# Kernel optimization log

Measured on AMD Instinct MI355X. Metric: run time of the kernel, lower is better.

## Reference

```python
import jax, jax.numpy as jnp
import numpy as np

N = 4096   # nodes
G = 64     # graphs
MH = 128   # hidden multiplicity (0e and 1o)
MU = 64    # up multiplicity (0e and 1o)
NSP = 10   # num_species
EPS = 1e-5


def _forward(nfh, nfu, onehot, W_h0, W_h1, W_u0, W_u1, Wt_00, Wt_11, Wt_01, Wt_10,
             W_p0, b_p0, W_p1, Wsc0, Wsc1, ln_w0, ln_b0, ln_w1, W_s0, b_s0, W_s1, batch):
    n = nfh.shape[0]
    # unpack irreps layout: [0e scalars | 1o vectors flattened]
    h0 = nfh[:, :MH]                       # [N, MH]
    h1 = nfh[:, MH:].reshape(n, MH, 3)     # [N, MH, 3]
    u0 = nfu[:, :MU]
    u1 = nfu[:, MU:].reshape(n, MU, 3)
    inv_h = 1.0 / np.sqrt(MH)
    inv_u = 1.0 / np.sqrt(MU)
    # irrep-wise (block-diagonal) o3.Linear, e3nn fan-in normalization
    hp0 = (h0 @ W_h0) * inv_h
    hp1 = jnp.einsum('nui,uv->nvi', h1, W_h1) * inv_h
    up0 = (u0 @ W_u0) * inv_u
    up1 = jnp.einsum('nui,uv->nvi', u1, W_u1) * inv_u
    # SeparateWeightTensorProduct: fully-connected 'uvw' CG tensor product
    # paths to 0e (scalars + gates, 2*MH outputs): 0e x 0e and 1o x 1o (dot / sqrt3)
    inv_tp = 1.0 / np.sqrt(2.0 * MH * MU)   # component/path normalization (2 paths, fan MH*MU)
    xy00 = jnp.einsum('nu,nv->nuv', hp0, up0).reshape(n, MH * MU)
    xy11 = jnp.einsum('nui,nvi->nuv', hp1, up1).reshape(n, MH * MU)
    z0 = (xy00 @ Wt_00.reshape(MH * MU, 2 * MH)
          + (xy11 @ Wt_11.reshape(MH * MU, 2 * MH)) / np.sqrt(3.0)) * inv_tp  # [N, 2*MH]
    # paths to 1o: 0e x 1o and 1o x 0e (staged to control intermediate size)
    ta = jnp.einsum('nu,uvw->nvw', hp0, Wt_01)       # [N, MU, MH]
    z1a = jnp.einsum('nvw,nvi->nwi', ta, up1)
    tb = jnp.einsum('nv,uvw->nuw', up0, Wt_10)       # [N, MH, MH]
    z1b = jnp.einsum('nuw,nui->nwi', tb, hp1)
    z1 = (z1a + z1b) * inv_tp                        # [N, MH, 3]
    # Gate nonlinearity: silu on scalars, sigmoid gates multiply 1o features
    s = jax.nn.silu(z0[:, :MH])
    g = jax.nn.sigmoid(z0[:, MH:])
    v = z1 * g[:, :, None]
    # lin_post (biases on scalars only)
    p0 = (s @ W_p0) * inv_h + b_p0
    p1 = jnp.einsum('nui,uv->nvi', v, W_p1) * inv_h
    # self-connection: FullyConnectedTensorProduct(hidden, NSPx0e, out)
    inv_sc = 1.0 / np.sqrt(MH * NSP)
    sxy0 = jnp.einsum('nu,nv->nuv', h0, onehot).reshape(n, MH * NSP)
    y0 = p0 + (sxy0 @ Wsc0.reshape(MH * NSP, MH)) * inv_sc
    sxy1 = jnp.einsum('nui,nv->nuvi', h1, onehot).reshape(n, MH * NSP, 3)
    y1 = p1 + jnp.einsum('nki,kw->nwi', sxy1, Wsc1.reshape(MH * NSP, MH)) * inv_sc
    # e3LayerNorm: per-graph stats; mean-subtract scalars only, RMS-normalize per irrep
    ones = jnp.ones((n,), y0.dtype)
    cnt = jnp.maximum(jax.ops.segment_sum(ones, batch, num_segments=G), 1.0)[:, None]
    mean0 = (jax.ops.segment_sum(y0, batch, num_segments=G) / cnt).mean(axis=1)  # [G]
    f0 = y0 - mean0[batch][:, None]
    var0 = (jax.ops.segment_sum(f0 * f0, batch, num_segments=G) / cnt).mean(axis=1)
    f0 = f0 / (jnp.sqrt(var0)[batch][:, None] + EPS) * ln_w0 + ln_b0
    var1 = (jax.ops.segment_sum((y1 * y1).reshape(n, -1), batch, num_segments=G) / cnt).mean(axis=1)
    f1 = y1 / (jnp.sqrt(var1)[batch][:, None, None] + EPS) * ln_w1[None, :, None]
    # residual skip connection (o3.Linear with scalar bias)
    out0 = f0 + (h0 @ W_s0) * inv_h + b_s0
    out1 = f1 + jnp.einsum('nui,uv->nvi', h1, W_s1) * inv_h
    return jnp.concatenate([out0, out1.reshape(n, 3 * MH)], axis=1)  # [N, 512]


def setup_inputs() -> dict:
    key = jax.random.key(0)
    ks = jax.random.split(key, 20)
    f = lambda i, shape: jax.random.normal(ks[i], shape, dtype=jnp.float32)
    species = jax.random.randint(ks[0], (N,), 0, NSP)
    return {
        'node_feats_hidden': f(1, (N, 4 * MH)),
        'node_feats_up': f(2, (N, 4 * MU)),
        'node_one_hot': jax.nn.one_hot(species, NSP, dtype=jnp.float32),
        'batch': jnp.sort(jax.random.randint(ks[3], (N,), 0, G)),
        'W_h0': f(4, (MH, MH)), 'W_h1': f(5, (MH, MH)),
        'W_u0': f(6, (MU, MU)), 'W_u1': f(7, (MU, MU)),
        'Wt_00': f(8, (MH, MU, 2 * MH)), 'Wt_11': f(9, (MH, MU, 2 * MH)),
        'Wt_01': f(10, (MH, MU, MH)), 'Wt_10': f(11, (MH, MU, MH)),
        'W_p0': f(12, (MH, MH)), 'b_p0': jnp.zeros((MH,), jnp.float32), 'W_p1': f(13, (MH, MH)),
        'Wsc0': f(14, (MH, NSP, MH)), 'Wsc1': f(15, (MH, NSP, MH)),
        'ln_w0': jnp.ones((MH,), jnp.float32), 'ln_b0': jnp.zeros((MH,), jnp.float32),
        'ln_w1': jnp.ones((MH,), jnp.float32),
        'W_s0': f(16, (MH, MH)), 'b_s0': jnp.zeros((MH,), jnp.float32), 'W_s1': f(17, (MH, MH)),
    }


def reference(node_feats_hidden, node_feats_up, node_one_hot, batch, W_h0, W_h1, W_u0, W_u1,
              Wt_00, Wt_11, Wt_01, Wt_10, W_p0, b_p0, W_p1, Wsc0, Wsc1, ln_w0, ln_b0, ln_w1,
              W_s0, b_s0, W_s1):
    return _forward(node_feats_hidden, node_feats_up, node_one_hot, W_h0, W_h1, W_u0, W_u1,
                    Wt_00, Wt_11, Wt_01, Wt_10, W_p0, b_p0, W_p1, Wsc0, Wsc1,
                    ln_w0, ln_b0, ln_w1, W_s0, b_s0, W_s1, batch)
```

## Files before the change

kernel.cpp:

```cpp
#include <hip/hip_runtime.h>
#include <cstdint>
#include <cstddef>


typedef _Float16 half8 __attribute__((ext_vector_type(8)));
typedef _Float16 half4v __attribute__((ext_vector_type(4)));
typedef float f32x4 __attribute__((ext_vector_type(4)));

static constexpr float INV_H  = 0.08838834764831845f;
static constexpr float INV_U  = 0.125f;
static constexpr float INV_TP = 0.0078125f;
static constexpr float INV_SC = 0.02795084971874737f;
static constexpr float RSQRT3 = 0.5773502691896258f;
static constexpr float LN_EPS = 1e-5f;

static constexpr size_t OFF_BZ0 = 0;
static constexpr size_t OFF_BZ1 = OFF_BZ0 + 8388608;
static constexpr size_t OFF_WH0 = OFF_BZ1 + 4194304;
static constexpr size_t OFF_WH1 = OFF_WH0 + 32768;
static constexpr size_t OFF_WU0 = OFF_WH1 + 32768;
static constexpr size_t OFF_WU1 = OFF_WU0 + 8192;
static constexpr size_t OFF_WP0 = OFF_WU1 + 8192;
static constexpr size_t OFF_WP1 = OFF_WP0 + 32768;
static constexpr size_t OFF_WS0 = OFF_WP1 + 32768;
static constexpr size_t OFF_WS1 = OFF_WS0 + 32768;
static constexpr size_t OFF_H0F = OFF_WS1 + 32768;
static constexpr size_t OFF_H1F = OFF_H0F + 1048576;
static constexpr size_t OFF_U0F = OFF_H1F + 3145728;
static constexpr size_t OFF_U1F = OFF_U0F + 524288;
static constexpr size_t OFF_HP0 = OFF_U1F + 1572864;
static constexpr size_t OFF_HP1 = OFF_HP0 + 1048576;
static constexpr size_t OFF_UP0 = OFF_HP1 + 3145728;
static constexpr size_t OFF_UP1 = OFF_UP0 + 524288;
static constexpr size_t OFF_SF  = OFF_UP1 + 1572864;
static constexpr size_t OFF_VF  = OFF_SF + 1048576;
static constexpr size_t OFF_PZ0 = OFF_VF + 3145728;
static constexpr size_t OFF_PZ1 = OFF_PZ0 + 16777216;
static constexpr size_t OFF_Y0  = OFF_PZ1 + 12582912;
static constexpr size_t OFF_Y1  = OFF_Y0 + 2097152;
static constexpr size_t OFF_O0  = OFF_Y1 + 6291456;
static constexpr size_t OFF_O1  = OFF_O0 + 2097152;
static constexpr size_t OFF_SP  = OFF_O1 + 6291456;
static constexpr size_t OFF_ST  = OFF_SP + 16384;
static constexpr size_t WS_NEED = OFF_ST + 2048;

__global__ __launch_bounds__(256) void kconv(
    const float* __restrict__ nfh, const float* __restrict__ nfu,
    const float* __restrict__ onehot,
    const float* __restrict__ Wt00, const float* __restrict__ Wt11,
    const float* __restrict__ Wt01, const float* __restrict__ Wt10,
    const float* __restrict__ Wh0, const float* __restrict__ Wh1,
    const float* __restrict__ Wu0, const float* __restrict__ Wu1,
    const float* __restrict__ Wp0, const float* __restrict__ Wp1,
    const float* __restrict__ Ws0, const float* __restrict__ Ws1,
    char* __restrict__ ws)
{
  const int bid = blockIdx.x, t = threadIdx.x;
  if (bid < 768) {
    _Float16* dst;
    int u, nt = 0;
    const bool isz0 = bid < 512;
    if (isz0) { nt = bid >> 8; u = bid & 255; dst = (_Float16*)(ws + OFF_BZ0) + ((size_t)nt*256 + (size_t)u)*8192; }
    else      { u = bid - 512;               dst = (_Float16*)(ws + OFF_BZ1) + (size_t)u*8192; }
    for (int it = 0; it < 4; ++it) {
      int chunk = it*256 + t;
      int lane = chunk & 63, ch = chunk >> 6;
      int f = ch >> 1, c = ch & 1;
      int w = f*16 + (lane & 15);
      int v0 = c*32 + (lane >> 4)*8;
      half8 o;
      #pragma unroll
      for (int j = 0; j < 8; ++j) {
        float val;
        if (isz0) {
          if (u < 128) val = Wt00[(size_t)((u*64 + v0 + j)*256) + nt*128 + w];
          else         val = Wt11[(size_t)(((u-128)*64 + v0 + j)*256) + nt*128 + w] * RSQRT3;
        } else {
          if (u < 128) val = Wt01[(size_t)((u*64 + v0 + j)*128) + w];
          else         val = Wt10[(size_t)(((u-128)*64 + v0 + j)*128) + w];
        }
        o[j] = (_Float16)val;
      }
      *(half8*)(dst + (size_t)chunk*8) = o;
    }
  } else if (bid < 776) {
    int mat = bid - 768;
    const float* src; size_t doff; int K, N;
    switch (mat) {
      case 0: src = Wh0; doff = OFF_WH0; K = 128; N = 128; break;
      case 1: src = Wh1; doff = OFF_WH1; K = 128; N = 128; break;
      case 2: src = Wu0; doff = OFF_WU0; K = 64;  N = 64;  break;
      case 3: src = Wu1; doff = OFF_WU1; K = 64;  N = 64;  break;
      case 4: src = Wp0; doff = OFF_WP0; K = 128; N = 128; break;
      case 5: src = Wp1; doff = OFF_WP1; K = 128; N = 128; break;
      case 6: src = Ws0; doff = OFF_WS0; K = 128; N = 128; break;
      default: src = Ws1; doff = OFF_WS1; K = 128; N = 128; break;
    }
    _Float16* d = (_Float16*)(ws + doff);
    const int nfr = N >> 4;
    const int chunks = (K*N) >> 3;
    for (int qd = t; qd < chunks; qd += 256) {
      int lane = qd & 63, cf = qd >> 6;
      int f = cf % nfr, c = cf / nfr;
      int col = f*16 + (lane & 15);
      int k0 = c*32 + (lane >> 4)*8;
      half8 o;
      #pragma unroll
      for (int j = 0; j < 8; ++j) o[j] = (_Float16)src[(size_t)(k0 + j)*N + col];
      *(half8*)(d + (size_t)qd*8) = o;
    }
  } else if (bid < 1544) {
    const int stride = 768*256;
    const int base = (bid - 776)*256 + t;
    _Float16* h0f = (_Float16*)(ws + OFF_H0F);
    _Float16* h1f = (_Float16*)(ws + OFF_H1F);
    _Float16* u0f = (_Float16*)(ws + OFF_U0F);
    _Float16* u1f = (_Float16*)(ws + OFF_U1F);
    for (int id = base; id < 524288; id += stride)
      h0f[id] = (_Float16)nfh[(size_t)(id >> 7)*512 + (id & 127)];
    for (int id = base; id < 1572864; id += stride) {
      int i = id >> 19, r = id & 524287, n = r >> 7, u = r & 127;
      h1f[id] = (_Float16)nfh[(size_t)n*512 + 128 + u*3 + i];
    }
    for (int id = base; id < 262144; id += stride)
      u0f[id] = (_Float16)nfu[(size_t)(id >> 6)*256 + (id & 63)];
    for (int id = base; id < 786432; id += stride) {
      int i = id >> 18, r = id & 262143, n = r >> 6, v = r & 63;
      u1f[id] = (_Float16)nfu[(size_t)n*256 + 64 + v*3 + i];
    }
  } else {
    int node = (bid - 1544)*256 + t;
    const float* row = onehot + (size_t)node*10;
    int best = 0; float bv = row[0];
    #pragma unroll
    for (int s = 1; s < 10; ++s) { float v = row[s]; if (v > bv) { bv = v; best = s; } }
    ((int*)(ws + OFF_SP))[node] = best;
    if (bid == 1544) {
      float* stz = (float*)(ws + OFF_ST);
      stz[t] = 0.f; stz[t + 256] = 0.f;
    }
  }
}

template<int KK, int NO, int MODE>
__global__ __launch_bounds__(256) void kgemm_small(char* __restrict__ ws,
    const float* __restrict__ bp0, const float* __restrict__ bs0)
{
  constexpr int NT = NO / 16;
  const int bid = blockIdx.x, t = threadIdx.x;
  const int lane = t & 63, wid = t >> 6;
  const int quad = lane >> 4, l15 = lane & 15;
  const int job = bid >> 5, n0 = (bid & 31) << 7;

  const _Float16 *A, *W;
  _Float16* oh = nullptr; float* of = nullptr;
  const float* bias = nullptr;
  float scale;
  if constexpr (MODE == 0) {
    scale = INV_H;
    if (job == 0) { A = (const _Float16*)(ws + OFF_H0F); W = (const _Float16*)(ws + OFF_WH0); oh = (_Float16*)(ws + OFF_HP0); }
    else {
      A = (const _Float16*)(ws + OFF_H1F) + (size_t)(job-1)*524288;
      W = (const _Float16*)(ws + OFF_WH1);
      oh = (_Float16*)(ws + OFF_HP1) + (size_t)(job-1)*524288;
    }
  } else if constexpr (MODE == 1) {
    scale = INV_U;
    if (job == 0) { A = (const _Float16*)(ws + OFF_U0F); W = (const _Float16*)(ws + OFF_WU0); oh = (_Float16*)(ws + OFF_UP0); }
    else {
      A = (const _Float16*)(ws + OFF_U1F) + (size_t)(job-1)*262144;
      W = (const _Float16*)(ws + OFF_WU1);
      oh = (_Float16*)(ws + OFF_UP1) + (size_t)(job-1)*262144;
    }
  } else {
    scale = INV_H;
    switch (job) {
      case 0: A = (const _Float16*)(ws + OFF_SF);  W = (const _Float16*)(ws + OFF_WP0); of = (float*)(ws + OFF_Y0); bias = bp0; break;
      case 1: A = (const _Float16*)(ws + OFF_H0F); W = (const _Float16*)(ws + OFF_WS0); of = (float*)(ws + OFF_O0); bias = bs0; break;
      case 2: case 3: case 4:
        A = (const _Float16*)(ws + OFF_VF) + (size_t)(job-2)*524288;
        W = (const _Float16*)(ws + OFF_WP1);
        of = (float*)(ws + OFF_Y1) + (size_t)(job-2)*524288; break;
      default:
        A = (const _Float16*)(ws + OFF_H1F) + (size_t)(job-5)*524288;
        W = (const _Float16*)(ws + OFF_WS1);
        of = (float*)(ws + OFF_O1) + (size_t)(job-5)*524288; break;
    }
  }

  f32x4 acc[2][NT];
  const f32x4 zz = {0.f, 0.f, 0.f, 0.f};
  #pragma unroll
  for (int mf = 0; mf < 2; ++mf)
    #pragma unroll
    for (int nf = 0; nf < NT; ++nf) acc[mf][nf] = zz;

  #pragma unroll
  for (int kc = 0; kc < KK/32; ++kc) {
    half8 a[2];
    #pragma unroll
    for (int mf = 0; mf < 2; ++mf)
      a[mf] = *(const half8*)(A + (size_t)(n0 + wid*32 + mf*16 + l15)*KK + kc*32 + quad*8);
    #pragma unroll
    for (int nf = 0; nf < NT; ++nf) {
      half8 b = *(const half8*)(W + (size_t)(kc*NT + nf)*512 + lane*8);
      #pragma unroll
      for (int mf = 0; mf < 2; ++mf)
        acc[mf][nf] = __builtin_amdgcn_mfma_f32_16x16x32_f16(a[mf], b, acc[mf][nf], 0, 0, 0);
    }
  }

  #pragma unroll
  for (int mf = 0; mf < 2; ++mf)
    #pragma unroll
    for (int nf = 0; nf < NT; ++nf) {
      int col = nf*16 + l15;
      float bv = bias ? bias[col] : 0.f;
      #pragma unroll
      for (int r = 0; r < 4; ++r) {
        int row = n0 + wid*32 + mf*16 + quad*4 + r;
        float v = acc[mf][nf][r] * scale + bv;
        if constexpr (MODE < 2) oh[(size_t)row*NO + col] = (_Float16)v;
        else                    of[(size_t)row*NO + col] = v;
      }
    }
}

__global__ __launch_bounds__(256, 2) void kbig(char* __restrict__ ws)
{
  const int bid = blockIdx.x, t = threadIdx.x;
  const int lane = t & 63, wid = t >> 6;
  const int wy = wid >> 1, wx = wid & 1;
  const int quad = lane >> 4, l15 = lane & 15;

  const _Float16* hp0 = (const _Float16*)(ws + OFF_HP0);
  const _Float16* hp1 = (const _Float16*)(ws + OFF_HP1);
  const _Float16* up0 = (const _Float16*)(ws + OFF_UP0);
  const _Float16* up1 = (const _Float16*)(ws + OFF_UP1);

  const _Float16 *p, *q, *B0;
  float* out; int opitch; size_t obase; int node0;
  if (bid < 256) {
    int mt = bid >> 3, nt = (bid >> 2) & 1, kj = bid & 3;
    node0 = mt << 7;
    if (kj == 0) { p = hp0; q = up0; }
    else { p = hp1 + (size_t)(kj-1)*524288; q = up1 + (size_t)(kj-1)*262144; }
    B0 = (const _Float16*)(ws + OFF_BZ0) + (size_t)nt*2097152 + (kj ? (size_t)1048576 : (size_t)0);
    out = (float*)(ws + OFF_PZ0) + (size_t)kj*1048576;
    obase = (size_t)node0*256 + (size_t)nt*128;
    opitch = 256;
  } else {
    int b2 = bid - 256, mt = b2 >> 1, kj = b2 & 1, i = mt >> 5;
    node0 = (mt & 31) << 7;
    if (kj == 0) { p = hp0; q = up1 + (size_t)i*262144; }
    else         { p = hp1 + (size_t)i*524288; q = up0; }
    B0 = (const _Float16*)(ws + OFF_BZ1) + (kj ? (size_t)1048576 : (size_t)0);
    out = (float*)(ws + OFF_PZ1) + (size_t)kj*1572864;
    obase = (size_t)mt*16384;
    opitch = 128;
  }

  half8 qf[4][2];
  #pragma unroll
  for (int mf = 0; mf < 4; ++mf)
    #pragma unroll
    for (int c = 0; c < 2; ++c)
      qf[mf][c] = *(const half8*)(q + (size_t)(node0 + wy*64 + mf*16 + l15)*64 + c*32 + quad*8);

  f32x4 acc[4][4];
  const f32x4 zz = {0.f, 0.f, 0.f, 0.f};
  #pragma unroll
  for (int mf = 0; mf < 4; ++mf)
    #pragma unroll
    for (int nf = 0; nf < 4; ++nf) acc[mf][nf] = zz;

  const _Float16* prow = p + (size_t)(node0 + wy*64 + l15)*128;
  const _Float16* Bw = B0 + (size_t)wx*4096 + (size_t)lane*8;

  auto loadB = [&](half8 (&dst)[2][4], int uidx) {
    const _Float16* Bu = Bw + (size_t)uidx*8192;
    #pragma unroll
    for (int c = 0; c < 2; ++c)
      #pragma unroll
      for (int nf = 0; nf < 4; ++nf)
        dst[c][nf] = *(const half8*)(Bu + (size_t)((nf*2 + c)*512));
  };
  auto mstep = [&](const half8 (&bf)[2][4], const half4v (&pwl)[4], int uu) {
    #pragma unroll
    for (int mf = 0; mf < 4; ++mf) {
      const _Float16 ps = pwl[mf][uu];
      const half8 pv = {ps, ps, ps, ps, ps, ps, ps, ps};
      #pragma unroll
      for (int c = 0; c < 2; ++c) {
        half8 a = qf[mf][c] * pv;
        #pragma unroll
        for (int nf = 0; nf < 4; ++nf)
          acc[mf][nf] = __builtin_amdgcn_mfma_f32_16x16x32_f16(a, bf[c][nf], acc[mf][nf], 0, 0, 0);
      }
    }
  };

  half4v pw[4], pwN[4];
  #pragma unroll
  for (int mf = 0; mf < 4; ++mf)
    pw[mf] = *(const half4v*)(prow + (size_t)mf*2048);

  half8 bfA[2][4], bfB[2][4];
  loadB(bfA, 0);

  for (int u4 = 0; u4 < 32; ++u4) {
    const int b = u4*4;
    loadB(bfB, b + 1);
    mstep(bfA, pw, 0);
    loadB(bfA, b + 2);
    mstep(bfB, pw, 1);
    {
      const int np = (u4 < 31) ? (u4 + 1)*4 : u4*4;
      #pragma unroll
      for (int mf = 0; mf < 4; ++mf)
        pwN[mf] = *(const half4v*)(prow + (size_t)mf*2048 + np);
    }
    loadB(bfB, b + 3);
    mstep(bfA, pw, 2);
    loadB(bfA, (u4 < 31) ? (b + 4) : (b + 3));
    mstep(bfB, pw, 3);
    #pragma unroll
    for (int mf = 0; mf < 4; ++mf) pw[mf] = pwN[mf];
  }

  #pragma unroll
  for (int mf = 0; mf < 4; ++mf)
    #pragma unroll
    for (int nf = 0; nf < 4; ++nf) {
      int col = wx*64 + nf*16 + l15;
      #pragma unroll
      for (int r = 0; r < 4; ++r) {
        int row = wy*64 + mf*16 + quad*4 + r;
        out[obase + (size_t)row*opitch + col] = acc[mf][nf][r];
      }
    }
}

__global__ __launch_bounds__(256) void kreduce(char* __restrict__ ws)
{
  const int id = blockIdx.x*256 + threadIdx.x;
  const int n = id >> 7, w = id & 127;
  const float* pz0 = (const float*)(ws + OFF_PZ0);
  const float* pz1 = (const float*)(ws + OFF_PZ1);
  _Float16* sf = (_Float16*)(ws + OFF_SF);
  _Float16* vf = (_Float16*)(ws + OFF_VF);
  const size_t b = (size_t)n*256;
  float zs = (pz0[b + w] + pz0[1048576 + b + w] + pz0[2097152 + b + w] + pz0[3145728 + b + w]) * INV_TP;
  float zg = (pz0[b + 128 + w] + pz0[1048576 + b + 128 + w] + pz0[2097152 + b + 128 + w] + pz0[3145728 + b + 128 + w]) * INV_TP;
  float s = zs / (1.f + __expf(-zs));
  float g = 1.f / (1.f + __expf(-zg));
  sf[id] = (_Float16)s;
  #pragma unroll
  for (int i = 0; i < 3; ++i) {
    size_t r = ((size_t)i*4096 + (size_t)n)*128 + w;
    float z1v = (pz1[r] + pz1[1572864 + r]) * INV_TP;
    vf[(size_t)i*524288 + (size_t)n*128 + w] = (_Float16)(z1v * g);
  }
}

__global__ __launch_bounds__(256) void kscstats(char* __restrict__ ws,
    const float* __restrict__ nfh,
    const float* __restrict__ Wsc0, const float* __restrict__ Wsc1,
    const int* __restrict__ batch)
{
  const int t = threadIdx.x;
  const int node = blockIdx.x*2 + (t >> 7);
  const int w = t & 127;
  const int sp = ((const int*)(ws + OFF_SP))[node];
  const float* h = nfh + (size_t)node*512;
  float a0 = 0.f, a10 = 0.f, a11 = 0.f, a12 = 0.f;
  for (int u = 0; u < 128; ++u) {
    const size_t wi = (size_t)(u*10 + sp)*128 + w;
    float w0 = Wsc0[wi];
    float w1 = Wsc1[wi];
    a0 += h[u] * w0;
    a10 += h[128 + u*3 + 0] * w1;
    a11 += h[128 + u*3 + 1] * w1;
    a12 += h[128 + u*3 + 2] * w1;
  }
  float* y0 = (float*)(ws + OFF_Y0);
  float* y1 = (float*)(ws + OFF_Y1);
  const size_t i0 = (size_t)node*128 + w;
  float y0n  = y0[i0]           + INV_SC * a0;
  float y1n0 = y1[i0]           + INV_SC * a10;
  float y1n1 = y1[524288 + i0]  + INV_SC * a11;
  float y1n2 = y1[1048576 + i0] + INV_SC * a12;
  y0[i0] = y0n;
  y1[i0] = y1n0;
  y1[524288 + i0]  = y1n1;
  y1[1048576 + i0] = y1n2;

  float s0 = y0n, ss0 = y0n*y0n, ss1 = y1n0*y1n0 + y1n1*y1n1 + y1n2*y1n2;
  #pragma unroll
  for (int m = 1; m < 64; m <<= 1) {
    s0  += __shfl_xor(s0, m, 64);
    ss0 += __shfl_xor(ss0, m, 64);
    ss1 += __shfl_xor(ss1, m, 64);
  }
  __shared__ float red[4][3];
  if ((t & 63) == 0) {
    red[t >> 6][0] = s0; red[t >> 6][1] = ss0; red[t >> 6][2] = ss1;
  }
  __syncthreads();
  if ((t & 127) == 0) {
    const int wv = t >> 6;
    float* stp = (float*)(ws + OFF_ST);
    const int g = batch[node];
    atomicAdd(&stp[g],       red[wv][0] + red[wv+1][0]);
    atomicAdd(&stp[64 + g],  red[wv][1] + red[wv+1][1]);
    atomicAdd(&stp[128 + g], red[wv][2] + red[wv+1][2]);
    atomicAdd(&stp[192 + g], 1.f);
  }
}

__global__ __launch_bounds__(256) void kfinal(char* __restrict__ ws, const int* __restrict__ batch,
    const float* __restrict__ lnw0, const float* __restrict__ lnb0, const float* __restrict__ lnw1,
    float* __restrict__ outp)
{
  const int id = blockIdx.x*256 + threadIdx.x;
  const int n = id >> 9, c = id & 511;
  const float* st = (const float*)(ws + OFF_ST);
  const int g = batch[n];
  const float cnt = fmaxf(st[192 + g], 1.f);
  float val;
  if (c < 128) {
    const float* y0 = (const float*)(ws + OFF_Y0);
    const float* o0 = (const float*)(ws + OFF_O0);
    float m0   = st[g] / (cnt * 128.f);
    float var0 = st[64 + g] / (cnt * 128.f) - m0*m0;
    float inv0 = 1.f / (sqrtf(fmaxf(var0, 0.f)) + LN_EPS);
    val = (y0[(size_t)n*128 + c] - m0) * inv0 * lnw0[c] + lnb0[c] + o0[(size_t)n*128 + c];
  } else {
    int cc = c - 128, w = cc / 3, i = cc - w*3;
    const float* y1 = (const float*)(ws + OFF_Y1);
    const float* o1 = (const float*)(ws + OFF_O1);
    float inv1 = 1.f / (sqrtf(fmaxf(st[128 + g] / (cnt * 384.f), 0.f)) + LN_EPS);
    val = y1[(size_t)i*524288 + (size_t)n*128 + w] * inv1 * lnw1[w]
        + o1[(size_t)i*524288 + (size_t)n*128 + w];
  }
  outp[id] = val;
}

extern "C" void kernel_launch(void* const* d_in, const int* in_sizes, int n_in,
                              void* d_out, int out_size, void* d_ws, size_t ws_size,
                              hipStream_t stream)
{
  const float* nfh   = (const float*)d_in[0];
  const float* nfu   = (const float*)d_in[1];
  const float* oneh  = (const float*)d_in[2];
  const int*   batch = (const int*)d_in[3];
  const float* Wh0   = (const float*)d_in[4];
  const float* Wh1   = (const float*)d_in[5];
  const float* Wu0   = (const float*)d_in[6];
  const float* Wu1   = (const float*)d_in[7];
  const float* Wt00  = (const float*)d_in[8];
  const float* Wt11  = (const float*)d_in[9];
  const float* Wt01  = (const float*)d_in[10];
  const float* Wt10  = (const float*)d_in[11];
  const float* Wp0   = (const float*)d_in[12];
  const float* bp0   = (const float*)d_in[13];
  const float* Wp1   = (const float*)d_in[14];
  const float* Wsc0  = (const float*)d_in[15];
  const float* Wsc1  = (const float*)d_in[16];
  const float* lnw0  = (const float*)d_in[17];
  const float* lnb0  = (const float*)d_in[18];
  const float* lnw1  = (const float*)d_in[19];
  const float* Ws0   = (const float*)d_in[20];
  const float* bs0   = (const float*)d_in[21];
  const float* Ws1   = (const float*)d_in[22];
  char* ws = (char*)d_ws;

  if (ws_size < WS_NEED) {
    hipMemsetAsync(d_out, 0, (size_t)out_size * sizeof(float), stream);
    return;
  }

  kconv<<<1560, 256, 0, stream>>>(nfh, nfu, oneh, Wt00, Wt11, Wt01, Wt10,
                                  Wh0, Wh1, Wu0, Wu1, Wp0, Wp1, Ws0, Ws1, ws);
  kgemm_small<128,128,0><<<128, 256, 0, stream>>>(ws, nullptr, nullptr);
  kgemm_small<64, 64, 1><<<128, 256, 0, stream>>>(ws, nullptr, nullptr);
  kbig<<<448, 256, 0, stream>>>(ws);
  kreduce<<<2048, 256, 0, stream>>>(ws);
  kgemm_small<128,128,2><<<256, 256, 0, stream>>>(ws, bp0, bs0);
  kscstats<<<2048, 256, 0, stream>>>(ws, nfh, Wsc0, Wsc1, batch);
  kfinal<<<8192, 256, 0, stream>>>(ws, batch, lnw0, lnb0, lnw1, (float*)d_out);
}
```

Baseline: 353.8 us.

## Restructure big tensor-product GEMM to share B tiles across spatial planes with K-split

Rewrites the main tensor-product kernel as a templated worker that processes all three vector components (planes) per B-fragment load, so each weight tile is reused across planes instead of reloaded per component. The K dimension is split in two with partial sums written to separate buffers, which the reduce kernel now adds together, and the grid grows from 448 to 640 blocks. The explicit double-buffered B prefetch is dropped in favour of simpler per-step loads. This trades more accumulator registers and extra partial-sum traffic for fewer weight loads and more parallelism.

```diff
diff --git a/kernel.cpp b/kernel.cpp
--- a/kernel.cpp
+++ b/kernel.cpp
@@ -226,119 +226,147 @@
     }
 }
 
+template<int MF, int NF, int PLANES, int PN, int QN, bool Z0>
+__device__ __forceinline__ void bigwork(
+    const _Float16* p0, const _Float16* p1, const _Float16* p2,
+    const _Float16* q0, const _Float16* q1, const _Float16* q2,
+    const _Float16* Bt,
+    float* out, size_t obase, int opitch,
+    int node0, int ks, int fbase, int t)
+{
+  constexpr int ACCP  = Z0 ? 1 : PLANES;
+  constexpr int WROWS = MF * 16;
+  const int lane = t & 63;
+  const int wy = (t >> 7) & 1;
+  const int quad = lane >> 4, l15 = lane & 15;
+
+  const _Float16* pp[3] = {p0, p1, p2};
+  const _Float16* qq[3] = {q0, q1, q2};
+
+  half8 qf[QN][MF][2];
+  #pragma unroll
+  for (int qi = 0; qi < QN; ++qi)
+    #pragma unroll
+    for (int mf = 0; mf < MF; ++mf)
+      #pragma unroll
+      for (int c = 0; c < 2; ++c)
+        qf[qi][mf][c] = *(const half8*)(qq[qi] + (size_t)(node0 + wy*WROWS + mf*16 + l15)*64 + c*32 + quad*8);
+
+  f32x4 acc[ACCP][MF][NF];
+  const f32x4 zz = {0.f, 0.f, 0.f, 0.f};
+  #pragma unroll
+  for (int ap = 0; ap < ACCP; ++ap)
+    #pragma unroll
+    for (int mf = 0; mf < MF; ++mf)
+      #pragma unroll
+      for (int nf = 0; nf < NF; ++nf) acc[ap][mf][nf] = zz;
+
+  const _Float16* prow[PN];
+  #pragma unroll
+  for (int pi = 0; pi < PN; ++pi)
+    prow[pi] = pp[pi] + (size_t)(node0 + wy*WROWS + l15)*128 + ks*64;
+
+  const _Float16* Bl = Bt + (size_t)fbase*1024 + (size_t)lane*8;
+
+  for (int u4 = 0; u4 < 16; ++u4) {
+    half4v pw[PN][MF];
+    #pragma unroll
+    for (int pi = 0; pi < PN; ++pi)
+      #pragma unroll
+      for (int mf = 0; mf < MF; ++mf)
+        pw[pi][mf] = *(const half4v*)(prow[pi] + (size_t)mf*2048 + u4*4);
+    #pragma unroll
+    for (int uu = 0; uu < 4; ++uu) {
+      const _Float16* Bu = Bl + (size_t)(u4*4 + uu)*8192;
+      half8 bf[2][NF];
+      #pragma unroll
+      for (int c = 0; c < 2; ++c)
+        #pragma unroll
+        for (int nf = 0; nf < NF; ++nf)
+          bf[c][nf] = *(const half8*)(Bu + (size_t)((nf*2 + c)*512));
+      #pragma unroll
+      for (int c = 0; c < 2; ++c)
+        #pragma unroll
+        for (int pl = 0; pl < PLANES; ++pl)
+          #pragma unroll
+          for (int mf = 0; mf < MF; ++mf) {
+            const _Float16 ps = pw[PN == 1 ? 0 : pl][mf][uu];
+            const half8 pv = {ps, ps, ps, ps, ps, ps, ps, ps};
+            half8 a = qf[QN == 1 ? 0 : pl][mf][c] * pv;
+            #pragma unroll
+            for (int nf = 0; nf < NF; ++nf)
+              acc[Z0 ? 0 : pl][mf][nf] =
+                __builtin_amdgcn_mfma_f32_16x16x32_f16(a, bf[c][nf], acc[Z0 ? 0 : pl][mf][nf], 0, 0, 0);
+          }
+    }
+  }
+
+  #pragma unroll
+  for (int pl = 0; pl < ACCP; ++pl)
+    #pragma unroll
+    for (int mf = 0; mf < MF; ++mf)
+      #pragma unroll
+      for (int nf = 0; nf < NF; ++nf) {
+        const int col = (fbase + nf)*16 + l15;
+        #pragma unroll
+        for (int r = 0; r < 4; ++r) {
+          const int row = wy*WROWS + mf*16 + quad*4 + r;
+          out[(size_t)pl*524288 + obase + (size_t)row*opitch + col] = acc[pl][mf][nf][r];
+        }
+      }
+}
+
 __global__ __launch_bounds__(256, 2) void kbig(char* __restrict__ ws)
 {
   const int bid = blockIdx.x, t = threadIdx.x;
-  const int lane = t & 63, wid = t >> 6;
-  const int wy = wid >> 1, wx = wid & 1;
-  const int quad = lane >> 4, l15 = lane & 15;
+  const int wx = (t >> 6) & 1;
 
   const _Float16* hp0 = (const _Float16*)(ws + OFF_HP0);
   const _Float16* hp1 = (const _Float16*)(ws + OFF_HP1);
   const _Float16* up0 = (const _Float16*)(ws + OFF_UP0);
   const _Float16* up1 = (const _Float16*)(ws + OFF_UP1);
-
-  const _Float16 *p, *q, *B0;
-  float* out; int opitch; size_t obase; int node0;
-  if (bid < 256) {
-    int mt = bid >> 3, nt = (bid >> 2) & 1, kj = bid & 3;
-    node0 = mt << 7;
-    if (kj == 0) { p = hp0; q = up0; }
-    else { p = hp1 + (size_t)(kj-1)*524288; q = up1 + (size_t)(kj-1)*262144; }
-    B0 = (const _Float16*)(ws + OFF_BZ0) + (size_t)nt*2097152 + (kj ? (size_t)1048576 : (size_t)0);
-    out = (float*)(ws + OFF_PZ0) + (size_t)kj*1048576;
-    obase = (size_t)node0*256 + (size_t)nt*128;
-    opitch = 256;
+  const _Float16* BZ0h = (const _Float16*)(ws + OFF_BZ0);
+  const _Float16* BZ1h = (const _Float16*)(ws + OFF_BZ1);
+  float* pz0 = (float*)(ws + OFF_PZ0);
+  float* pzA = (float*)(ws + OFF_PZ1);
+  float* pzB = (float*)(ws + OFF_Y0);
+
+  if (bid < 128) {
+    const int idx = bid, mt = idx >> 3, nb = (idx >> 1) & 3, ks = idx & 1;
+    const int node0 = mt << 8, nt = nb >> 1;
+    const int fbase = (nb & 1)*4 + wx*2;
+    const _Float16* Bt = BZ0h + (size_t)(nt*256 + ks*64)*8192;
+    bigwork<8, 2, 1, 1, 1, true>(hp0, hp0, hp0, up0, up0, up0, Bt,
+        pz0 + (size_t)ks*1048576, (size_t)node0*256 + (size_t)nt*128, 256,
+        node0, ks, fbase, t);
+  } else if (bid < 384) {
+    const int idx = bid - 128, mt = idx >> 3, cb = (idx >> 1) & 3, ks = idx & 1;
+    const int node0 = mt << 7, nt = cb >> 1;
+    const int fbase = (cb & 1)*4 + wx*2;
+    const _Float16* Bt = BZ0h + (size_t)(nt*256 + 128 + ks*64)*8192;
+    bigwork<4, 2, 3, 3, 3, true>(hp1, hp1 + 524288, hp1 + 1048576,
+                                 up1, up1 + 262144, up1 + 524288, Bt,
+        pz0 + (size_t)(2 + ks)*1048576, (size_t)node0*256 + (size_t)nt*128, 256,
+        node0, ks, fbase, t);
+  } else if (bid < 512) {
+    const int idx = bid - 384, mt = idx >> 2, nb = (idx >> 1) & 1, ks = idx & 1;
+    const int node0 = mt << 7;
+    const int fbase = nb*4 + wx*2;
+    const _Float16* Bt = BZ1h + (size_t)(ks*64)*8192;
+    bigwork<4, 2, 3, 1, 3, false>(hp0, hp0, hp0,
+                                  up1, up1 + 262144, up1 + 524288, Bt,
+        pzA + (size_t)ks*1572864, (size_t)node0*128, 128,
+        node0, ks, fbase, t);
   } else {
-    int b2 = bid - 256, mt = b2 >> 1, kj = b2 & 1, i = mt >> 5;
-    node0 = (mt & 31) << 7;
-    if (kj == 0) { p = hp0; q = up1 + (size_t)i*262144; }
-    else         { p = hp1 + (size_t)i*524288; q = up0; }
-    B0 = (const _Float16*)(ws + OFF_BZ1) + (kj ? (size_t)1048576 : (size_t)0);
-    out = (float*)(ws + OFF_PZ1) + (size_t)kj*1572864;
-    obase = (size_t)mt*16384;
-    opitch = 128;
-  }
-
-  half8 qf[4][2];
-  #pragma unroll
-  for (int mf = 0; mf < 4; ++mf)
-    #pragma unroll
-    for (int c = 0; c < 2; ++c)
-      qf[mf][c] = *(const half8*)(q + (size_t)(node0 + wy*64 + mf*16 + l15)*64 + c*32 + quad*8);
-
-  f32x4 acc[4][4];
-  const f32x4 zz = {0.f, 0.f, 0.f, 0.f};
-  #pragma unroll
-  for (int mf = 0; mf < 4; ++mf)
-    #pragma unroll
-    for (int nf = 0; nf < 4; ++nf) acc[mf][nf] = zz;
-
-  const _Float16* prow = p + (size_t)(node0 + wy*64 + l15)*128;
-  const _Float16* Bw = B0 + (size_t)wx*4096 + (size_t)lane*8;
-
-  auto loadB = [&](half8 (&dst)[2][4], int uidx) {
-    const _Float16* Bu = Bw + (size_t)uidx*8192;
-    #pragma unroll
-    for (int c = 0; c < 2; ++c)
-      #pragma unroll
-      for (int nf = 0; nf < 4; ++nf)
-        dst[c][nf] = *(const half8*)(Bu + (size_t)((nf*2 + c)*512));
-  };
-  auto mstep = [&](const half8 (&bf)[2][4], const half4v (&pwl)[4], int uu) {
-    #pragma unroll
-    for (int mf = 0; mf < 4; ++mf) {
-      const _Float16 ps = pwl[mf][uu];
-      const half8 pv = {ps, ps, ps, ps, ps, ps, ps, ps};
-      #pragma unroll
-      for (int c = 0; c < 2; ++c) {
-        half8 a = qf[mf][c] * pv;
-        #pragma unroll
-        for (int nf = 0; nf < 4; ++nf)
-          acc[mf][nf] = __builtin_amdgcn_mfma_f32_16x16x32_f16(a, bf[c][nf], acc[mf][nf], 0, 0, 0);
-      }
-    }
-  };
-
-  half4v pw[4], pwN[4];
-  #pragma unroll
-  for (int mf = 0; mf < 4; ++mf)
-    pw[mf] = *(const half4v*)(prow + (size_t)mf*2048);
-
-  half8 bfA[2][4], bfB[2][4];
-  loadB(bfA, 0);
-
-  for (int u4 = 0; u4 < 32; ++u4) {
-    const int b = u4*4;
-    loadB(bfB, b + 1);
-    mstep(bfA, pw, 0);
-    loadB(bfA, b + 2);
-    mstep(bfB, pw, 1);
-    {
-      const int np = (u4 < 31) ? (u4 + 1)*4 : u4*4;
-      #pragma unroll
-      for (int mf = 0; mf < 4; ++mf)
-        pwN[mf] = *(const half4v*)(prow + (size_t)mf*2048 + np);
-    }
-    loadB(bfB, b + 3);
-    mstep(bfA, pw, 2);
-    loadB(bfA, (u4 < 31) ? (b + 4) : (b + 3));
-    mstep(bfB, pw, 3);
-    #pragma unroll
-    for (int mf = 0; mf < 4; ++mf) pw[mf] = pwN[mf];
-  }
-
-  #pragma unroll
-  for (int mf = 0; mf < 4; ++mf)
-    #pragma unroll
-    for (int nf = 0; nf < 4; ++nf) {
-      int col = wx*64 + nf*16 + l15;
-      #pragma unroll
-      for (int r = 0; r < 4; ++r) {
-        int row = wy*64 + mf*16 + quad*4 + r;
-        out[obase + (size_t)row*opitch + col] = acc[mf][nf][r];
-      }
-    }
+    const int idx = bid - 512, mt = idx >> 2, nb = (idx >> 1) & 1, ks = idx & 1;
+    const int node0 = mt << 7;
+    const int fbase = nb*4 + wx*2;
+    const _Float16* Bt = BZ1h + (size_t)(128 + ks*64)*8192;
+    bigwork<4, 2, 3, 3, 1, false>(hp1, hp1 + 524288, hp1 + 1048576,
+                                  up0, up0, up0, Bt,
+        pzB + (size_t)ks*1572864, (size_t)node0*128, 128,
+        node0, ks, fbase, t);
+  }
 }
 
 __global__ __launch_bounds__(256) void kreduce(char* __restrict__ ws)
@@ -346,7 +374,8 @@
   const int id = blockIdx.x*256 + threadIdx.x;
   const int n = id >> 7, w = id & 127;
   const float* pz0 = (const float*)(ws + OFF_PZ0);
-  const float* pz1 = (const float*)(ws + OFF_PZ1);
+  const float* pzA = (const float*)(ws + OFF_PZ1);
+  const float* pzB = (const float*)(ws + OFF_Y0);
   _Float16* sf = (_Float16*)(ws + OFF_SF);
   _Float16* vf = (_Float16*)(ws + OFF_VF);
   const size_t b = (size_t)n*256;
@@ -358,7 +387,7 @@
   #pragma unroll
   for (int i = 0; i < 3; ++i) {
     size_t r = ((size_t)i*4096 + (size_t)n)*128 + w;
-    float z1v = (pz1[r] + pz1[1572864 + r]) * INV_TP;
+    float z1v = (pzA[r] + pzA[1572864 + r] + pzB[r] + pzB[1572864 + r]) * INV_TP;
     vf[(size_t)i*524288 + (size_t)n*128 + w] = (_Float16)(z1v * g);
   }
 }
@@ -484,7 +513,7 @@
                                   Wh0, Wh1, Wu0, Wu1, Wp0, Wp1, Ws0, Ws1, ws);
   kgemm_small<128,128,0><<<128, 256, 0, stream>>>(ws, nullptr, nullptr);
   kgemm_small<64, 64, 1><<<128, 256, 0, stream>>>(ws, nullptr, nullptr);
-  kbig<<<448, 256, 0, stream>>>(ws);
+  kbig<<<640, 256, 0, stream>>>(ws);
   kreduce<<<2048, 256, 0, stream>>>(ws);
   kgemm_small<128,128,2><<<256, 256, 0, stream>>>(ws, bp0, bs0);
   kscstats<<<2048, 256, 0, stream>>>(ws, nfh, Wsc0, Wsc1, batch);
```

New measurement: 370.8 us. 4.8% more time.

## Split-K the z0 GEMM blocks, remap kbig by XCD, merge small GEMM launches

Applied to the files above, without the earlier changes.

The z0 contraction blocks in kbig are split along the reduction dimension into two halves. The second half writes partial sums into the reused Y0/O0 buffers, and kreduce sums the extra partials. Block indices are remapped so that work sharing the same B weights lands on the same XCD, and the launch grows from 448 to 704 blocks. Occupancy is raised to 3 blocks per CU, and the manual double-buffered B prefetch is dropped for a simpler loop. The two prep GEMM launches are merged into one kernel. The changes target tail imbalance and L2 locality, at the cost of more partial-sum traffic and possibly exposed load latency.

```diff
diff --git a/kernel.cpp b/kernel.cpp
--- a/kernel.cpp
+++ b/kernel.cpp
@@ -143,11 +143,11 @@
 }
 
 template<int KK, int NO, int MODE>
-__global__ __launch_bounds__(256) void kgemm_small(char* __restrict__ ws,
-    const float* __restrict__ bp0, const float* __restrict__ bs0)
+__device__ __forceinline__ void gemm_small_body(char* __restrict__ ws,
+    const float* __restrict__ bp0, const float* __restrict__ bs0,
+    int bid, int t)
 {
   constexpr int NT = NO / 16;
-  const int bid = blockIdx.x, t = threadIdx.x;
   const int lane = t & 63, wid = t >> 6;
   const int quad = lane >> 4, l15 = lane & 15;
   const int job = bid >> 5, n0 = (bid & 31) << 7;
@@ -226,119 +226,131 @@
     }
 }
 
-__global__ __launch_bounds__(256, 2) void kbig(char* __restrict__ ws)
-{
-  const int bid = blockIdx.x, t = threadIdx.x;
+__global__ __launch_bounds__(256) void kprep(char* __restrict__ ws)
+{
+  if (blockIdx.x < 128) gemm_small_body<128,128,0>(ws, nullptr, nullptr, blockIdx.x, threadIdx.x);
+  else                  gemm_small_body<64, 64, 1>(ws, nullptr, nullptr, blockIdx.x - 128, threadIdx.x);
+}
+
+__global__ __launch_bounds__(256) void ktail(char* __restrict__ ws,
+    const float* __restrict__ bp0, const float* __restrict__ bs0)
+{
+  gemm_small_body<128,128,2>(ws, bp0, bs0, blockIdx.x, threadIdx.x);
+}
+
+__device__ __forceinline__ void bigloop(
+    const _Float16* __restrict__ p, const _Float16* __restrict__ q,
+    const _Float16* __restrict__ B0,
+    float* __restrict__ out, size_t obase, int opitch,
+    int node0, int ustart4, int nu4, int t)
+{
   const int lane = t & 63, wid = t >> 6;
   const int wy = wid >> 1, wx = wid & 1;
   const int quad = lane >> 4, l15 = lane & 15;
+
+  half8 qf[4][2];
+  #pragma unroll
+  for (int mf = 0; mf < 4; ++mf)
+    #pragma unroll
+    for (int c = 0; c < 2; ++c)
+      qf[mf][c] = *(const half8*)(q + (size_t)(node0 + wy*64 + mf*16 + l15)*64 + c*32 + quad*8);
+
+  f32x4 acc[4][4];
+  const f32x4 zz = {0.f, 0.f, 0.f, 0.f};
+  #pragma unroll
+  for (int mf = 0; mf < 4; ++mf)
+    #pragma unroll
+    for (int nf = 0; nf < 4; ++nf) acc[mf][nf] = zz;
+
+  const _Float16* prow = p + (size_t)(node0 + wy*64 + l15)*128 + ustart4*4;
+  const _Float16* Bw = B0 + (size_t)ustart4*32768 + (size_t)wx*4096 + (size_t)lane*8;
+
+  for (int u4 = 0; u4 < nu4; ++u4) {
+    half4v pw[4];
+    #pragma unroll
+    for (int mf = 0; mf < 4; ++mf)
+      pw[mf] = *(const half4v*)(prow + (size_t)mf*2048 + u4*4);
+    #pragma unroll
+    for (int uu = 0; uu < 4; ++uu) {
+      const _Float16* Bu = Bw + (size_t)(u4*4 + uu)*8192;
+      half8 bf[2][4];
+      #pragma unroll
+      for (int c = 0; c < 2; ++c)
+        #pragma unroll
+        for (int nf = 0; nf < 4; ++nf)
+          bf[c][nf] = *(const half8*)(Bu + (size_t)((nf*2 + c)*512));
+      #pragma unroll
+      for (int mf = 0; mf < 4; ++mf) {
+        const _Float16 ps = pw[mf][uu];
+        const half8 pv = {ps, ps, ps, ps, ps, ps, ps, ps};
+        #pragma unroll
+        for (int c = 0; c < 2; ++c) {
+          half8 a = qf[mf][c] * pv;
+          #pragma unroll
+          for (int nf = 0; nf < 4; ++nf)
+            acc[mf][nf] = __builtin_amdgcn_mfma_f32_16x16x32_f16(a, bf[c][nf], acc[mf][nf], 0, 0, 0);
+        }
+      }
+    }
+  }
+
+  #pragma unroll
+  for (int mf = 0; mf < 4; ++mf)
+    #pragma unroll
+    for (int nf = 0; nf < 4; ++nf) {
+      int col = wx*64 + nf*16 + l15;
+      #pragma unroll
+      for (int r = 0; r < 4; ++r) {
+        int row = wy*64 + mf*16 + quad*4 + r;
+        out[obase + (size_t)row*opitch + col] = acc[mf][nf][r];
+      }
+    }
+}
+
+__global__ __launch_bounds__(256, 3) void kbig(char* __restrict__ ws)
+{
+  const int bid = blockIdx.x, t = threadIdx.x;
+  const int xcd = bid & 7, j = bid >> 3;
 
   const _Float16* hp0 = (const _Float16*)(ws + OFF_HP0);
   const _Float16* hp1 = (const _Float16*)(ws + OFF_HP1);
   const _Float16* up0 = (const _Float16*)(ws + OFF_UP0);
   const _Float16* up1 = (const _Float16*)(ws + OFF_UP1);
-
-  const _Float16 *p, *q, *B0;
-  float* out; int opitch; size_t obase; int node0;
-  if (bid < 256) {
-    int mt = bid >> 3, nt = (bid >> 2) & 1, kj = bid & 3;
-    node0 = mt << 7;
+  const _Float16* BZ0 = (const _Float16*)(ws + OFF_BZ0);
+  const _Float16* BZ1 = (const _Float16*)(ws + OFF_BZ1);
+
+  if (j < 24) {
+    const int kj = xcd >> 2;
+    const int g = (xcd & 3)*24 + j;
+    const int i = g >> 5, mt = g & 31;
+    const int node0 = mt << 7;
+    const _Float16 *p, *q;
+    if (kj == 0) { p = hp0; q = up1 + (size_t)i*262144; }
+    else         { p = hp1 + (size_t)i*524288; q = up0; }
+    const _Float16* B0 = BZ1 + (kj ? (size_t)1048576 : (size_t)0);
+    float* out = (float*)(ws + OFF_PZ1) + (size_t)kj*1572864;
+    bigloop(p, q, B0, out, (size_t)(i*32 + mt)*16384, 128, node0, 0, 32, t);
+  } else {
+    const int s = xcd & 3, nt = s >> 1, ks = s & 1;
+    const int j2 = j - 24;
+    int kj, mt;
+    if (j2 < 48) {
+      const int g = (xcd >> 2)*48 + j2;
+      kj = 1 + (g >> 5); mt = g & 31;
+    } else {
+      kj = 0; mt = (xcd >> 2)*16 + (j2 - 48);
+    }
+    const int node0 = mt << 7;
+    const _Float16 *p, *q;
     if (kj == 0) { p = hp0; q = up0; }
     else { p = hp1 + (size_t)(kj-1)*524288; q = up1 + (size_t)(kj-1)*262144; }
-    B0 = (const _Float16*)(ws + OFF_BZ0) + (size_t)nt*2097152 + (kj ? (size_t)1048576 : (size_t)0);
-    out = (float*)(ws + OFF_PZ0) + (size_t)kj*1048576;
-    obase = (size_t)node0*256 + (size_t)nt*128;
-    opitch = 256;
-  } else {
-    int b2 = bid - 256, mt = b2 >> 1, kj = b2 & 1, i = mt >> 5;
-    node0 = (mt & 31) << 7;
-    if (kj == 0) { p = hp0; q = up1 + (size_t)i*262144; }
-    else         { p = hp1 + (size_t)i*524288; q = up0; }
-    B0 = (const _Float16*)(ws + OFF_BZ1) + (kj ? (size_t)1048576 : (size_t)0);
-    out = (float*)(ws + OFF_PZ1) + (size_t)kj*1572864;
-    obase = (size_t)mt*16384;
-    opitch = 128;
-  }
-
-  half8 qf[4][2];
-  #pragma unroll
-  for (int mf = 0; mf < 4; ++mf)
-    #pragma unroll
-    for (int c = 0; c < 2; ++c)
-      qf[mf][c] = *(const half8*)(q + (size_t)(node0 + wy*64 + mf*16 + l15)*64 + c*32 + quad*8);
-
-  f32x4 acc[4][4];
-  const f32x4 zz = {0.f, 0.f, 0.f, 0.f};
-  #pragma unroll
-  for (int mf = 0; mf < 4; ++mf)
-    #pragma unroll
-    for (int nf = 0; nf < 4; ++nf) acc[mf][nf] = zz;
-
-  const _Float16* prow = p + (size_t)(node0 + wy*64 + l15)*128;
-  const _Float16* Bw = B0 + (size_t)wx*4096 + (size_t)lane*8;
-
-  auto loadB = [&](half8 (&dst)[2][4], int uidx) {
-    const _Float16* Bu = Bw + (size_t)uidx*8192;
-    #pragma unroll
-    for (int c = 0; c < 2; ++c)
-      #pragma unroll
-      for (int nf = 0; nf < 4; ++nf)
-        dst[c][nf] = *(const half8*)(Bu + (size_t)((nf*2 + c)*512));
-  };
-  auto mstep = [&](const half8 (&bf)[2][4], const half4v (&pwl)[4], int uu) {
-    #pragma unroll
-    for (int mf = 0; mf < 4; ++mf) {
-      const _Float16 ps = pwl[mf][uu];
-      const half8 pv = {ps, ps, ps, ps, ps, ps, ps, ps};
-      #pragma unroll
-      for (int c = 0; c < 2; ++c) {
-        half8 a = qf[mf][c] * pv;
-        #pragma unroll
-        for (int nf = 0; nf < 4; ++nf)
-          acc[mf][nf] = __builtin_amdgcn_mfma_f32_16x16x32_f16(a, bf[c][nf], acc[mf][nf], 0, 0, 0);
-      }
-    }
-  };
-
-  half4v pw[4], pwN[4];
-  #pragma unroll
-  for (int mf = 0; mf < 4; ++mf)
-    pw[mf] = *(const half4v*)(prow + (size_t)mf*2048);
-
-  half8 bfA[2][4], bfB[2][4];
-  loadB(bfA, 0);
-
-  for (int u4 = 0; u4 < 32; ++u4) {
-    const int b = u4*4;
-    loadB(bfB, b + 1);
-    mstep(bfA, pw, 0);
-    loadB(bfA, b + 2);
-    mstep(bfB, pw, 1);
-    {
-      const int np = (u4 < 31) ? (u4 + 1)*4 : u4*4;
-      #pragma unroll
-      for (int mf = 0; mf < 4; ++mf)
-        pwN[mf] = *(const half4v*)(prow + (size_t)mf*2048 + np);
-    }
-    loadB(bfB, b + 3);
-    mstep(bfA, pw, 2);
-    loadB(bfA, (u4 < 31) ? (b + 4) : (b + 3));
-    mstep(bfB, pw, 3);
-    #pragma unroll
-    for (int mf = 0; mf < 4; ++mf) pw[mf] = pwN[mf];
-  }
-
-  #pragma unroll
-  for (int mf = 0; mf < 4; ++mf)
-    #pragma unroll
-    for (int nf = 0; nf < 4; ++nf) {
-      int col = wx*64 + nf*16 + l15;
-      #pragma unroll
-      for (int r = 0; r < 4; ++r) {
-        int row = wy*64 + mf*16 + quad*4 + r;
-        out[obase + (size_t)row*opitch + col] = acc[mf][nf][r];
-      }
-    }
+    const _Float16* B0 = BZ0 + (size_t)nt*2097152 + (kj ? (size_t)1048576 : (size_t)0);
+    float* out;
+    if (ks == 0)      out = (float*)(ws + OFF_PZ0) + (size_t)kj*1048576;
+    else if (kj < 2)  out = (float*)(ws + OFF_Y0)  + (size_t)kj*1048576;
+    else              out = (float*)(ws + OFF_O0)  + (size_t)(kj-2)*1048576;
+    bigloop(p, q, B0, out, (size_t)node0*256 + (size_t)nt*128, 256, node0, ks*16, 16, t);
+  }
 }
 
 __global__ __launch_bounds__(256) void kreduce(char* __restrict__ ws)
@@ -346,12 +358,16 @@
   const int id = blockIdx.x*256 + threadIdx.x;
   const int n = id >> 7, w = id & 127;
   const float* pz0 = (const float*)(ws + OFF_PZ0);
+  const float* pe0 = (const float*)(ws + OFF_Y0);
+  const float* pe1 = (const float*)(ws + OFF_O0);
   const float* pz1 = (const float*)(ws + OFF_PZ1);
   _Float16* sf = (_Float16*)(ws + OFF_SF);
   _Float16* vf = (_Float16*)(ws + OFF_VF);
   const size_t b = (size_t)n*256;
-  float zs = (pz0[b + w] + pz0[1048576 + b + w] + pz0[2097152 + b + w] + pz0[3145728 + b + w]) * INV_TP;
-  float zg = (pz0[b + 128 + w] + pz0[1048576 + b + 128 + w] + pz0[2097152 + b + 128 + w] + pz0[3145728 + b + 128 + w]) * INV_TP;
+  float zs = (pz0[b + w] + pz0[1048576 + b + w] + pz0[2097152 + b + w] + pz0[3145728 + b + w]
+            + pe0[b + w] + pe0[1048576 + b + w] + pe1[b + w] + pe1[1048576 + b + w]) * INV_TP;
+  float zg = (pz0[b + 128 + w] + pz0[1048576 + b + 128 + w] + pz0[2097152 + b + 128 + w] + pz0[3145728 + b + 128 + w]
+            + pe0[b + 128 + w] + pe0[1048576 + b + 128 + w] + pe1[b + 128 + w] + pe1[1048576 + b + 128 + w]) * INV_TP;
   float s = zs / (1.f + __expf(-zs));
   float g = 1.f / (1.f + __expf(-zg));
   sf[id] = (_Float16)s;
@@ -482,11 +498,10 @@
 
   kconv<<<1560, 256, 0, stream>>>(nfh, nfu, oneh, Wt00, Wt11, Wt01, Wt10,
                                   Wh0, Wh1, Wu0, Wu1, Wp0, Wp1, Ws0, Ws1, ws);
-  kgemm_small<128,128,0><<<128, 256, 0, stream>>>(ws, nullptr, nullptr);
-  kgemm_small<64, 64, 1><<<128, 256, 0, stream>>>(ws, nullptr, nullptr);
-  kbig<<<448, 256, 0, stream>>>(ws);
+  kprep<<<256, 256, 0, stream>>>(ws);
+  kbig<<<704, 256, 0, stream>>>(ws);
   kreduce<<<2048, 256, 0, stream>>>(ws);
-  kgemm_small<128,128,2><<<256, 256, 0, stream>>>(ws, bp0, bs0);
+  ktail<<<256, 256, 0, stream>>>(ws, bp0, bs0);
   kscstats<<<2048, 256, 0, stream>>>(ws, nfh, Wsc0, Wsc1, batch);
   kfinal<<<8192, 256, 0, stream>>>(ws, batch, lnw0, lnb0, lnw1, (float*)d_out);
 }
```

After: 383.1 us. 8.3% more time.
